# Optimization experiments

Measured on AMD Instinct MI355X. Metric: run time of the kernel, lower is better.

## Reference

```python
import jax, jax.numpy as jnp
import numpy as np

N = 20000          # nodes
E = 320000         # edges (avg degree 16)
FS = 1000          # feature_size (resnet feature width)
IN = 250 + FS + 250 + 85 * 3  # 1755, actual concat width


def setup_inputs() -> dict:
    key = jax.random.key(0)
    ks = jax.random.split(key, 16)
    # structured node feature matrix x: [layer_id | resnet(1000) | rel_size | rgb(3)]
    layer = jax.random.randint(ks[0], (N, 1), 1, 4).astype(jnp.float32)      # {1,2,3}
    resnet = jax.random.normal(ks[1], (N, FS), jnp.float32)
    rel = jax.random.uniform(ks[2], (N, 1), jnp.float32)                      # [0,1] -> idx 0..10
    colors = jax.random.randint(ks[3], (N, 3), 0, 256).astype(jnp.float32)
    x = jnp.concatenate([layer, resnet, rel, colors], axis=1)  # [N,1005]
    edge_index = jax.random.randint(ks[4], (2, E), 0, N)
    edge_attr = jax.random.uniform(ks[5], (E,), jnp.float32)

    def lin(k, fi, fo):
        return jax.random.normal(k, (fi, fo), jnp.float32) / np.sqrt(fi).astype(np.float32)

    return {
        "x": x,
        "edge_index": edge_index,
        "edge_attr": edge_attr,
        "layer_table": jax.random.normal(ks[6], (3, 250), jnp.float32),
        "rel_table": jax.random.normal(ks[7], (11, 250), jnp.float32),
        "color_table": jax.random.normal(ks[8], (256, 85), jnp.float32),
        "W1": lin(ks[9], IN, 512), "b1": jnp.zeros((512,), jnp.float32),
        "W2": lin(ks[10], 512, 256), "b2": jnp.zeros((256,), jnp.float32),
        "W3": lin(ks[11], 256, 64), "b3": jnp.zeros((64,), jnp.float32),
        "Wp": lin(ks[12], 64, 3), "bp": jnp.zeros((3,), jnp.float32),
    }


def _gcn_conv(h, src, dst, ew, W, b):
    # PyG GCNConv: h' = D^{-1/2} (A + I) D^{-1/2} (h W) + b, with edge weights ew
    h = h @ W
    deg = jax.ops.segment_sum(ew, dst, num_segments=N) + 1.0  # +1 for self-loop weight
    dinv = jnp.where(deg > 0.0, jax.lax.rsqrt(deg), 0.0)
    norm = dinv[src] * ew * dinv[dst]                          # [E]
    agg = jax.ops.segment_sum(h[src] * norm[:, None], dst, num_segments=N)
    agg = agg + h * (dinv * dinv)[:, None]                     # self-loop term
    return agg + b


def reference(x, edge_index, edge_attr, layer_table, rel_table, color_table,
              W1, b1, W2, b2, W3, b3, Wp, bp):
    src, dst = edge_index[0], edge_index[1]
    li = (x[:, 0] - 1.0).astype(jnp.int32)                      # layer id 0..2
    le = layer_table[li]                                        # [N,250]
    resnet = x[:, 1:FS + 1]                                     # [N,1000]
    ri = jnp.round(jnp.abs(x[:, FS + 1]) * 10.0).astype(jnp.int32)
    re = rel_table[ri]                                          # [N,250]
    ci = x[:, -3:].astype(jnp.int32)
    ce = color_table[ci].reshape(x.shape[0], -1)                # [N,255]
    h = jnp.concatenate([le, resnet, re, ce], axis=1)           # [N,1755]

    lrelu = lambda v: jax.nn.leaky_relu(v, 0.01)
    h = lrelu(_gcn_conv(h, src, dst, edge_attr, W1, b1))
    h = lrelu(_gcn_conv(h, src, dst, edge_attr, W2, b2))
    h = lrelu(_gcn_conv(h, src, dst, edge_attr, W3, b3))
    return h @ Wp + bp                                          # [N,3]
```

## Files before the change

kernel.cpp:

```cpp
#include <hip/hip_runtime.h>
#include <hip/hip_bf16.h>

#define NNODES 20000
#define NEDGES 320000
#define XW 1005
#define MP 20096

typedef __attribute__((ext_vector_type(8))) short short8;
typedef __attribute__((ext_vector_type(4))) float f32x4;
typedef __attribute__((ext_vector_type(4))) unsigned short u16x4;

typedef const __attribute__((address_space(1))) short8* g8cp;

__device__ inline void split1(float v, unsigned short& h, unsigned short& l) {
    unsigned u = __float_as_uint(v);
    h = (unsigned short)(u >> 16);
    float hf = __uint_as_float(u & 0xffff0000u);
    l = (unsigned short)(__float_as_uint(v - hf) >> 16);
}

#define PB_EDGE  1250
#define PB_IDX   1329
#define PB_A1    21329
#define PB_BT1   21841
#define PB_BT2   21969
#define PB_BT3   21985
#define PB_TAB   23549

__device__ inline void bt_split_body(int g, const float* __restrict__ W, int ldw,
                                     int koff, int K, int Kp, int Ncols,
                                     unsigned short* __restrict__ Bh,
                                     unsigned short* __restrict__ Bl) {
    int kp4 = Kp >> 2;
    if (g >= Ncols * kp4) return;
    int n = g / kp4, c4 = (g % kp4) << 2;
    u16x4 h, l;
#pragma unroll
    for (int i = 0; i < 4; ++i) {
        int k = c4 + i;
        float v = (k < K) ? W[(size_t)(koff + k) * ldw + n] : 0.0f;
        unsigned short hh, ll;
        split1(v, hh, ll);
        h[i] = (short)hh; l[i] = (short)ll;
    }
    *(u16x4*)&Bh[(size_t)n * Kp + c4] = h;
    *(u16x4*)&Bl[(size_t)n * Kp + c4] = l;
}

__global__ __launch_bounds__(256) void prep_kernel(
    const float* __restrict__ x, const int* __restrict__ ei, const float* __restrict__ ea,
    const float* __restrict__ layer_table, const float* __restrict__ rel_table,
    const float* __restrict__ color_table,
    const float* __restrict__ W1, const float* __restrict__ W2, const float* __restrict__ W3,
    float* __restrict__ deg, int* __restrict__ counts, int* __restrict__ idx8,
    unsigned short* __restrict__ A1h, unsigned short* __restrict__ A1l,
    unsigned short* __restrict__ Bt1h, unsigned short* __restrict__ Bt1l,
    unsigned short* __restrict__ Bt2h, unsigned short* __restrict__ Bt2l,
    unsigned short* __restrict__ Bt3h, unsigned short* __restrict__ Bt3l,
    float* __restrict__ T) {
    const int b = blockIdx.x;
    const int t = threadIdx.x;
    if (b < PB_EDGE) {
        int e = b * 256 + t;
        if (e >= NEDGES) return;
        int dst = ei[NEDGES + e];
        atomicAdd(&deg[dst], ea[e]);
        atomicAdd(&counts[dst], 1);
    } else if (b < PB_IDX) {
        int i = (b - PB_EDGE) * 256 + t;
        if (i >= NNODES) return;
        const float* r = x + (size_t)i * XW;
        idx8[i * 8 + 0] = (int)(r[0] - 1.0f);
        idx8[i * 8 + 1] = (int)rintf(fabsf(r[1001]) * 10.0f);
        idx8[i * 8 + 2] = (int)r[1002];
        idx8[i * 8 + 3] = (int)r[1003];
        idx8[i * 8 + 4] = (int)r[1004];
    } else if (b < PB_A1) {
        int row = b - PB_IDX;
        int c4 = t << 2;
        const float* xp = x + (size_t)row * XW + 1 + c4;
        u16x4 h, l;
#pragma unroll
        for (int i = 0; i < 4; ++i) {
            float v = (c4 + i < 1000) ? xp[i] : 0.0f;
            unsigned short hh, ll;
            split1(v, hh, ll);
            h[i] = (short)hh; l[i] = (short)ll;
        }
        *(u16x4*)&A1h[(size_t)row * 1024 + c4] = h;
        *(u16x4*)&A1l[(size_t)row * 1024 + c4] = l;
    } else if (b < PB_BT1) {
        bt_split_body((b - PB_A1) * 256 + t, W1, 512, 250, 1000, 1024, 512, Bt1h, Bt1l);
    } else if (b < PB_BT2) {
        bt_split_body((b - PB_BT1) * 256 + t, W2, 256, 0, 512, 512, 256, Bt2h, Bt2l);
    } else if (b < PB_BT3) {
        bt_split_body((b - PB_BT2) * 256 + t, W3, 64, 0, 256, 256, 64, Bt3h, Bt3l);
    } else {
        int g = (b - PB_BT3) * 256 + t;
        if (g >= 782 * 512) return;
        int row = g >> 9, col = g & 511;
        float acc = 0.0f;
        if (row < 3) {
            for (int k = 0; k < 250; ++k)
                acc += layer_table[row * 250 + k] * W1[(size_t)k * 512 + col];
        } else if (row < 14) {
            int r = row - 3;
            for (int k = 0; k < 250; ++k)
                acc += rel_table[r * 250 + k] * W1[(size_t)(1250 + k) * 512 + col];
        } else {
            int r = row - 14;
            int j = r >> 8, v = r & 255;
            int base = 1500 + 85 * j;
            for (int k = 0; k < 85; ++k)
                acc += color_table[v * 85 + k] * W1[(size_t)(base + k) * 512 + col];
        }
        T[(size_t)row * 512 + col] = acc;
    }
}


__global__ __launch_bounds__(1024) void scan_p1_kernel(const int* __restrict__ counts,
                                                       int* __restrict__ bsum,
                                                       const float* __restrict__ deg,
                                                       float* __restrict__ dinv, int n) {
    int b = blockIdx.x;
    if (b < 20) {
        __shared__ int ws[16];
        int t = threadIdx.x, lane = t & 63, wid = t >> 6;
        int i = b * 1024 + t;
        int v = (i < n) ? counts[i] : 0;
#pragma unroll
        for (int d = 32; d; d >>= 1) v += __shfl_down(v, d, 64);
        if (lane == 0) ws[wid] = v;
        __syncthreads();
        if (wid == 0) {
            int s = (lane < 16) ? ws[lane] : 0;
#pragma unroll
            for (int d = 8; d; d >>= 1) s += __shfl_down(s, d, 64);
            if (lane == 0) bsum[b] = s;
        }
    } else {
        int i = (b - 20) * 1024 + threadIdx.x;
        if (i < n) { float d = deg[i] + 1.0f; dinv[i] = 1.0f / sqrtf(d); }
    }
}

__global__ void scan_p2_kernel(const int* __restrict__ bsum, int* __restrict__ boffs,
                               int* __restrict__ offs, int n, int nb) {
    int lane = threadIdx.x;
    int v = (lane < nb) ? bsum[lane] : 0;
    int xv = v;
#pragma unroll
    for (int d = 1; d < 64; d <<= 1) {
        int u = __shfl_up(xv, d, 64);
        if (lane >= d) xv += u;
    }
    if (lane < nb) boffs[lane] = xv - v;
    if (lane == nb - 1) offs[n] = xv;
}

__global__ __launch_bounds__(1024) void scan_p3_kernel(const int* __restrict__ counts,
                                                       const int* __restrict__ boffs,
                                                       int* __restrict__ offs, int n) {
    __shared__ int wsum[16], wpre[16];
    int t = threadIdx.x, lane = t & 63, wid = t >> 6;
    int i = blockIdx.x * 1024 + t;
    int v = (i < n) ? counts[i] : 0;
    int xv = v;
#pragma unroll
    for (int d = 1; d < 64; d <<= 1) {
        int u = __shfl_up(xv, d, 64);
        if (lane >= d) xv += u;
    }
    if (lane == 63) wsum[wid] = xv;
    __syncthreads();
    if (wid == 0) {
        int s = (lane < 16) ? wsum[lane] : 0;
#pragma unroll
        for (int d = 1; d < 16; d <<= 1) {
            int u = __shfl_up(s, d, 64);
            if (lane >= d) s += u;
        }
        if (lane < 16) wpre[lane] = s;
    }
    __syncthreads();
    int prefix = boffs[blockIdx.x] + (wid > 0 ? wpre[wid - 1] : 0);
    if (i < n) offs[i] = prefix + xv - v;
}

__global__ void scatter_kernel(const int* __restrict__ ei, const float* __restrict__ ea,
                               const float* __restrict__ dinv, const int* __restrict__ offs,
                               int* __restrict__ cursor, int* __restrict__ csr_src,
                               float* __restrict__ csr_norm, int E) {
    int e = blockIdx.x * 256 + threadIdx.x;
    if (e >= E) return;
    int src = ei[e];
    int dst = ei[E + e];
    int slot = offs[dst] + atomicAdd(&cursor[dst], 1);
    csr_src[slot] = src;
    csr_norm[slot] = dinv[src] * ea[e] * dinv[dst];
}


template <int BN, int NCB, bool EMB>
__global__ __launch_bounds__(256, 3) void gemm_areg_kernel(
    const unsigned short* __restrict__ Ah, const unsigned short* __restrict__ Al, int Kp,
    const unsigned short* __restrict__ Bh, const unsigned short* __restrict__ Bl,
    float* __restrict__ C, int ldc, int M,
    const float* __restrict__ T, const int* __restrict__ idx8) {
    constexpr int NT = BN / 32;
    constexpr int BJ = BN / 64;
    __shared__ __align__(16) unsigned short sBh[2][BN * 32];
    __shared__ __align__(16) unsigned short sBl[2][BN * 32];

    const int t = threadIdx.x;
    const int lane = t & 63;
    const int w = t >> 6;
    const int wr = w >> 1, wc = w & 1;
    const int l15 = lane & 15, quad = lane >> 4;

    const int total = gridDim.x;
    const int per = total >> 3;
    const int bid = blockIdx.x;
    const int tile = (bid < (per << 3)) ? ((bid & 7) * per + (bid >> 3)) : bid;
    const int row0 = (tile / NCB) * 128;
    const int col0 = (tile % NCB) * BN;

    const int si_r = lane >> 2;
    const int si_s = lane & 3;
    const int schunk = si_s ^ ((si_r >> 1) & 3);
    const int sw = (quad ^ ((l15 >> 1) & 3)) * 8;

    const unsigned short* pAh[4]; const unsigned short* pAl[4];
#pragma unroll
    for (int mt = 0; mt < 4; ++mt) {
        int r = row0 + wr * 64 + mt * 16 + l15;
        size_t o = (size_t)r * Kp + quad * 8;
        pAh[mt] = Ah + o; pAl[mt] = Al + o;
    }

    const unsigned short* gB[BJ][2];
    int boff[BJ];
#pragma unroll
    for (int j = 0; j < BJ; ++j) {
        int rb = w * (BN / 4) + j * 16 + si_r;
        size_t e = (size_t)(col0 + rb) * Kp + schunk * 8;
        gB[j][0] = Bh + e; gB[j][1] = Bl + e;
        boff[j] = (w * (BN / 4) + j * 16 + si_r) * 32 + si_s * 8;
    }

    f32x4 acc[4][NT];
#pragma unroll
    for (int i = 0; i < 4; ++i)
#pragma unroll
        for (int j = 0; j < NT; ++j)
            acc[i][j] = (f32x4){0.f, 0.f, 0.f, 0.f};

    const int nit = Kp / 32;

    short8 a_h[4], a_l[4];
#pragma unroll
    for (int mt = 0; mt < 4; ++mt) {
        a_h[mt] = *(g8cp)(const void*)(pAh[mt]);
        a_l[mt] = *(g8cp)(const void*)(pAl[mt]);
    }
    short8 pB[BJ][2];
#pragma unroll
    for (int j = 0; j < BJ; ++j) {
        pB[j][0] = *(g8cp)(const void*)(gB[j][0]);
        pB[j][1] = *(g8cp)(const void*)(gB[j][1]);
    }
#pragma unroll
    for (int j = 0; j < BJ; ++j) {
        *(short8*)&sBh[0][boff[j]] = pB[j][0];
        *(short8*)&sBl[0][boff[j]] = pB[j][1];
    }
#pragma unroll
    for (int j = 0; j < BJ; ++j) {
        pB[j][0] = *(g8cp)(const void*)(gB[j][0] + 32);
        pB[j][1] = *(g8cp)(const void*)(gB[j][1] + 32);
    }
    __builtin_amdgcn_s_waitcnt(0xC07F);
    __builtin_amdgcn_s_barrier();
    __builtin_amdgcn_sched_barrier(0);

    for (int kt = 0; kt < nit; ++kt) {
        const int cur = kt & 1, nxt = cur ^ 1;
        const int kbn = (kt + 1 < nit) ? (kt + 1) * 32 : 0;
#pragma unroll
        for (int j = 0; j < BJ; ++j) {
            *(short8*)&sBh[nxt][boff[j]] = pB[j][0];
            *(short8*)&sBl[nxt][boff[j]] = pB[j][1];
        }
        {
            const int kb2 = (kt + 2 < nit) ? (kt + 2) * 32 : 0;
#pragma unroll
            for (int j = 0; j < BJ; ++j) {
                pB[j][0] = *(g8cp)(const void*)(gB[j][0] + kb2);
                pB[j][1] = *(g8cp)(const void*)(gB[j][1] + kb2);
            }
        }
        __builtin_amdgcn_s_waitcnt(0xC07F);
        __builtin_amdgcn_s_barrier();
        __builtin_amdgcn_sched_barrier(0);

        short8 fbh[NT], fbl[NT];
#pragma unroll
        for (int nt = 0; nt < NT; ++nt) {
            int off = (wc * (BN / 2) + nt * 16 + l15) * 32 + sw;
            fbh[nt] = *(const short8*)&sBh[cur][off];
            fbl[nt] = *(const short8*)&sBl[cur][off];
        }
#pragma unroll
        for (int mt = 0; mt < 4; ++mt) {
#pragma unroll
            for (int nt = 0; nt < NT; ++nt)
                acc[mt][nt] = __builtin_amdgcn_mfma_f32_16x16x32_bf16(a_h[mt], fbh[nt], acc[mt][nt], 0, 0, 0);
#pragma unroll
            for (int nt = 0; nt < NT; ++nt)
                acc[mt][nt] = __builtin_amdgcn_mfma_f32_16x16x32_bf16(a_h[mt], fbl[nt], acc[mt][nt], 0, 0, 0);
#pragma unroll
            for (int nt = 0; nt < NT; ++nt)
                acc[mt][nt] = __builtin_amdgcn_mfma_f32_16x16x32_bf16(a_l[mt], fbh[nt], acc[mt][nt], 0, 0, 0);
            a_h[mt] = *(g8cp)(const void*)(pAh[mt] + kbn);
            a_l[mt] = *(g8cp)(const void*)(pAl[mt] + kbn);
        }
    }

#pragma unroll
    for (int mt = 0; mt < 4; ++mt)
#pragma unroll
        for (int r = 0; r < 4; ++r) {
            int row = row0 + wr * 64 + mt * 16 + quad * 4 + r;
            if (row >= M) continue;
            if (EMB) {
                const int* ix = idx8 + row * 8;
                const float* t0 = T + (size_t)ix[0] * 512;
                const float* t1 = T + (size_t)(3 + ix[1]) * 512;
                const float* t2 = T + (size_t)(14 + ix[2]) * 512;
                const float* t3 = T + (size_t)(270 + ix[3]) * 512;
                const float* t4 = T + (size_t)(526 + ix[4]) * 512;
#pragma unroll
                for (int nt = 0; nt < NT; ++nt) {
                    int col = col0 + wc * (BN / 2) + nt * 16 + l15;
                    float e = t0[col] + t1[col] + t2[col] + t3[col] + t4[col];
                    C[(size_t)row * ldc + col] = acc[mt][nt][r] + e;
                }
            } else {
#pragma unroll
                for (int nt = 0; nt < NT; ++nt) {
                    int col = col0 + wc * (BN / 2) + nt * 16 + l15;
                    C[(size_t)row * ldc + col] = acc[mt][nt][r];
                }
            }
        }
}


template <int F, int CW, bool SPLIT, bool PROJ>
__global__ __launch_bounds__(256) void agg_cols_kernel(
    const float* __restrict__ H, const float* __restrict__ dinv,
    const int* __restrict__ offs, const int* __restrict__ csr_src,
    const float* __restrict__ csr_norm, const float* __restrict__ bias,
    float* __restrict__ outf, unsigned short* __restrict__ Hh,
    unsigned short* __restrict__ Hl,
    const float* __restrict__ Wp, const float* __restrict__ bp, int n_nodes) {
    constexpr int LPN = CW / 4;
    constexpr int NPB = 256 / LPN;
    constexpr int NCH = F / CW;
    constexpr int ECAP = 2048;
    __shared__ int   se[ECAP];
    __shared__ float sn[ECAP];

    const int chunk = blockIdx.x & (NCH - 1);
    const int nb    = blockIdx.x / NCH;
    const int n0 = nb * NPB;
    const int n1 = min(n0 + NPB, n_nodes);
    if (n0 >= n_nodes) return;

    const int estart = offs[n0];
    const int eend   = offs[n1];
    const int ecnt   = eend - estart;
    const bool inlds = (ecnt <= ECAP);
    if (inlds) {
        for (int i = threadIdx.x; i < ecnt; i += 256) {
            se[i] = csr_src[estart + i];
            sn[i] = csr_norm[estart + i];
        }
    }
    __syncthreads();

    const int n = n0 + threadIdx.x / LPN;
    if (n >= n_nodes) return;
    const int lane = threadIdx.x % LPN;
    const int c = chunk * CW + lane * 4;

    float di = dinv[n];
    float s = di * di;
    float4 h = *(const float4*)(H + (size_t)n * F + c);
    float4 acc = make_float4(h.x * s, h.y * s, h.z * s, h.w * s);
    int e0 = offs[n], e1 = offs[n + 1];
    if (inlds) {
        for (int e = e0 - estart; e < e1 - estart; ++e) {
            int src = se[e];
            float w = sn[e];
            float4 v = *(const float4*)(H + (size_t)src * F + c);
            acc.x += v.x * w; acc.y += v.y * w; acc.z += v.z * w; acc.w += v.w * w;
        }
    } else {
        for (int e = e0; e < e1; ++e) {
            int src = csr_src[e];
            float w = csr_norm[e];
            float4 v = *(const float4*)(H + (size_t)src * F + c);
            acc.x += v.x * w; acc.y += v.y * w; acc.z += v.z * w; acc.w += v.w * w;
        }
    }
    float4 b = *(const float4*)(bias + c);
    acc.x += b.x; acc.y += b.y; acc.z += b.z; acc.w += b.w;
    acc.x = acc.x > 0.f ? acc.x : 0.01f * acc.x;
    acc.y = acc.y > 0.f ? acc.y : 0.01f * acc.y;
    acc.z = acc.z > 0.f ? acc.z : 0.01f * acc.z;
    acc.w = acc.w > 0.f ? acc.w : 0.01f * acc.w;
    if (PROJ) {
        float p[3];
#pragma unroll
        for (int j = 0; j < 3; ++j)
            p[j] = acc.x * Wp[(c + 0) * 3 + j] + acc.y * Wp[(c + 1) * 3 + j] +
                   acc.z * Wp[(c + 2) * 3 + j] + acc.w * Wp[(c + 3) * 3 + j];
#pragma unroll
        for (int d = 1; d < LPN; d <<= 1) {
#pragma unroll
            for (int j = 0; j < 3; ++j)
                p[j] += __shfl_xor(p[j], d, 64);
        }
        if (lane == 0) {
#pragma unroll
            for (int j = 0; j < 3; ++j)
                outf[n * 3 + j] = p[j] + bp[j];
        }
    } else if (SPLIT) {
        u16x4 hh, ll;
        unsigned short a, bb;
        split1(acc.x, a, bb); hh[0] = (short)a; ll[0] = (short)bb;
        split1(acc.y, a, bb); hh[1] = (short)a; ll[1] = (short)bb;
        split1(acc.z, a, bb); hh[2] = (short)a; ll[2] = (short)bb;
        split1(acc.w, a, bb); hh[3] = (short)a; ll[3] = (short)bb;
        *(u16x4*)(Hh + (size_t)n * F + c) = hh;
        *(u16x4*)(Hl + (size_t)n * F + c) = ll;
    } else {
        *(float4*)(outf + (size_t)n * F + c) = acc;
    }
}


static inline size_t aln(size_t v) { return (v + 255) & ~(size_t)255; }

extern "C" void kernel_launch(void* const* d_in, const int* in_sizes, int n_in,
                              void* d_out, int out_size, void* d_ws, size_t ws_size,
                              hipStream_t stream) {
    const float* x           = (const float*)d_in[0];
    const int*   edge_index  = (const int*)d_in[1];
    const float* edge_attr   = (const float*)d_in[2];
    const float* layer_table = (const float*)d_in[3];
    const float* rel_table   = (const float*)d_in[4];
    const float* color_table = (const float*)d_in[5];
    const float* W1 = (const float*)d_in[6];
    const float* b1 = (const float*)d_in[7];
    const float* W2 = (const float*)d_in[8];
    const float* b2 = (const float*)d_in[9];
    const float* W3 = (const float*)d_in[10];
    const float* b3 = (const float*)d_in[11];
    const float* Wp = (const float*)d_in[12];
    const float* bp = (const float*)d_in[13];
    float* out = (float*)d_out;

    const int N = NNODES, E = NEDGES;

    char* p = (char*)d_ws;
    float* deg      = (float*)p;
    int*   counts   = (int*)(p + (size_t)N * 4);
    int*   cursor   = (int*)(p + (size_t)N * 8);     p += aln((size_t)N * 12);
    float* dinv     = (float*)p; p += aln((size_t)N * 4);
    float* T        = (float*)p; p += aln((size_t)782 * 512 * 4);
    float* csr_norm = (float*)p; p += aln((size_t)E * 4);
    float* C        = (float*)p; p += aln((size_t)MP * 512 * 4);
    unsigned short* BIG = (unsigned short*)p; p += aln((size_t)MP * 2048 * 2);
    unsigned short* Bt1h = (unsigned short*)p; p += aln((size_t)512 * 1024 * 2);
    unsigned short* Bt1l = (unsigned short*)p; p += aln((size_t)512 * 1024 * 2);
    unsigned short* Bt2h = (unsigned short*)p; p += aln((size_t)256 * 512 * 2);
    unsigned short* Bt2l = (unsigned short*)p; p += aln((size_t)256 * 512 * 2);
    unsigned short* Bt3h = (unsigned short*)p; p += aln((size_t)64 * 256 * 2);
    unsigned short* Bt3l = (unsigned short*)p; p += aln((size_t)64 * 256 * 2);
    int*   csr_src  = (int*)p;   p += aln((size_t)E * 4);
    int*   idx8     = (int*)p;   p += aln((size_t)N * 8 * 4);
    int*   offs     = (int*)p;   p += aln((size_t)(N + 1) * 4);
    int*   bsum     = (int*)p;   p += aln((size_t)32 * 4);
    int*   boffs    = (int*)p;   p += aln((size_t)32 * 4);

    unsigned short* A1h = BIG;
    unsigned short* A1l = BIG + (size_t)MP * 1024;
    unsigned short* H2h = BIG;
    unsigned short* H2l = BIG + (size_t)MP * 512;
    unsigned short* H3h = BIG + (size_t)MP * 1024;
    unsigned short* H3l = BIG + (size_t)MP * 1024 + (size_t)MP * 256;

    hipMemsetAsync(deg, 0, (size_t)N * 12, stream);

    prep_kernel<<<PB_TAB, 256, 0, stream>>>(
        x, edge_index, edge_attr, layer_table, rel_table, color_table,
        W1, W2, W3, deg, counts, idx8,
        A1h, A1l, Bt1h, Bt1l, Bt2h, Bt2l, Bt3h, Bt3l, T);

    scan_p1_kernel<<<40, 1024, 0, stream>>>(counts, bsum, deg, dinv, N);
    scan_p2_kernel<<<1, 64, 0, stream>>>(bsum, boffs, offs, N, 20);
    scan_p3_kernel<<<20, 1024, 0, stream>>>(counts, boffs, offs, N);
    scatter_kernel<<<(E + 255) / 256, 256, 0, stream>>>(edge_index, edge_attr, dinv, offs,
                                                        cursor, csr_src, csr_norm, E);

    const int nrb = MP / 128;

    {
        gemm_areg_kernel<128, 4, true><<<nrb * 4, 256, 0, stream>>>(
            A1h, A1l, 1024, Bt1h, Bt1l, C, 512, N, T, idx8);
        int nblocks = (N + 15) / 16;
        agg_cols_kernel<512, 64, true, false><<<8 * nblocks, 256, 0, stream>>>(
            C, dinv, offs, csr_src, csr_norm, b1, nullptr, H2h, H2l, nullptr, nullptr, N);
    }
    {
        gemm_areg_kernel<128, 2, false><<<nrb * 2, 256, 0, stream>>>(
            H2h, H2l, 512, Bt2h, Bt2l, C, 256, N, nullptr, nullptr);
        int nblocks = (N + 31) / 32;
        agg_cols_kernel<256, 32, true, false><<<8 * nblocks, 256, 0, stream>>>(
            C, dinv, offs, csr_src, csr_norm, b2, nullptr, H3h, H3l, nullptr, nullptr, N);
    }
    {
        gemm_areg_kernel<64, 1, false><<<nrb, 256, 0, stream>>>(
            H3h, H3l, 256, Bt3h, Bt3l, C, 64, N, nullptr, nullptr);
        int nblocks = (N + 15) / 16;
        agg_cols_kernel<64, 64, false, true><<<nblocks, 256, 0, stream>>>(
            C, dinv, offs, csr_src, csr_norm, b3, out, nullptr, nullptr, Wp, bp, N);
    }
}
```

Baseline: 527.0 us.

## Stage A tiles through shared memory with 64-row GEMM blocks

Replaces the GEMM kernel, which kept A fragments in registers loaded straight from global memory and double-buffered B in LDS, with a 64-row block tile. Both A and B are now staged through single-buffered LDS, and each wave computes a 32-row by BN/2 subtile. The smaller tile doubles the block count and cuts per-thread accumulator and register use, which is meant to raise occupancy and spread work better across CUs. In exchange it drops the B double buffering, adding a second barrier per k-step, and each B tile is reused over fewer rows, so more total B traffic is loaded.

```diff
diff --git a/kernel.cpp b/kernel.cpp
--- a/kernel.cpp
+++ b/kernel.cpp
@@ -203,15 +203,17 @@
 
 
 template <int BN, int NCB, bool EMB>
-__global__ __launch_bounds__(256, 3) void gemm_areg_kernel(
+__global__ __launch_bounds__(256, 3) void gemm_bm64_kernel(
     const unsigned short* __restrict__ Ah, const unsigned short* __restrict__ Al, int Kp,
     const unsigned short* __restrict__ Bh, const unsigned short* __restrict__ Bl,
     float* __restrict__ C, int ldc, int M,
     const float* __restrict__ T, const int* __restrict__ idx8) {
     constexpr int NT = BN / 32;
     constexpr int BJ = BN / 64;
-    __shared__ __align__(16) unsigned short sBh[2][BN * 32];
-    __shared__ __align__(16) unsigned short sBl[2][BN * 32];
+    __shared__ __align__(16) unsigned short sAh[64 * 32];
+    __shared__ __align__(16) unsigned short sAl[64 * 32];
+    __shared__ __align__(16) unsigned short sBh[BN * 32];
+    __shared__ __align__(16) unsigned short sBl[BN * 32];
 
     const int t = threadIdx.x;
     const int lane = t & 63;
@@ -223,7 +225,7 @@
     const int per = total >> 3;
     const int bid = blockIdx.x;
     const int tile = (bid < (per << 3)) ? ((bid & 7) * per + (bid >> 3)) : bid;
-    const int row0 = (tile / NCB) * 128;
+    const int row0 = (tile / NCB) * 64;
     const int col0 = (tile % NCB) * BN;
 
     const int si_r = lane >> 2;
@@ -231,14 +233,14 @@
     const int schunk = si_s ^ ((si_r >> 1) & 3);
     const int sw = (quad ^ ((l15 >> 1) & 3)) * 8;
 
-    const unsigned short* pAh[4]; const unsigned short* pAl[4];
-#pragma unroll
-    for (int mt = 0; mt < 4; ++mt) {
-        int r = row0 + wr * 64 + mt * 16 + l15;
-        size_t o = (size_t)r * Kp + quad * 8;
-        pAh[mt] = Ah + o; pAl[mt] = Al + o;
-    }
-
+    const unsigned short* gA[2];
+    int aoff;
+    {
+        int ra = w * 16 + si_r;
+        size_t e = (size_t)(row0 + ra) * Kp + schunk * 8;
+        gA[0] = Ah + e; gA[1] = Al + e;
+        aoff = (w * 16 + si_r) * 32 + si_s * 8;
+    }
     const unsigned short* gB[BJ][2];
     int boff[BJ];
 #pragma unroll
@@ -249,89 +251,82 @@
         boff[j] = (w * (BN / 4) + j * 16 + si_r) * 32 + si_s * 8;
     }
 
-    f32x4 acc[4][NT];
-#pragma unroll
-    for (int i = 0; i < 4; ++i)
+    f32x4 acc[2][NT];
+#pragma unroll
+    for (int i = 0; i < 2; ++i)
 #pragma unroll
         for (int j = 0; j < NT; ++j)
             acc[i][j] = (f32x4){0.f, 0.f, 0.f, 0.f};
 
     const int nit = Kp / 32;
 
-    short8 a_h[4], a_l[4];
-#pragma unroll
-    for (int mt = 0; mt < 4; ++mt) {
-        a_h[mt] = *(g8cp)(const void*)(pAh[mt]);
-        a_l[mt] = *(g8cp)(const void*)(pAl[mt]);
-    }
-    short8 pB[BJ][2];
+    short8 pA[2], pB[BJ][2];
+    pA[0] = *(g8cp)(const void*)(gA[0]);
+    pA[1] = *(g8cp)(const void*)(gA[1]);
 #pragma unroll
     for (int j = 0; j < BJ; ++j) {
         pB[j][0] = *(g8cp)(const void*)(gB[j][0]);
         pB[j][1] = *(g8cp)(const void*)(gB[j][1]);
     }
-#pragma unroll
-    for (int j = 0; j < BJ; ++j) {
-        *(short8*)&sBh[0][boff[j]] = pB[j][0];
-        *(short8*)&sBl[0][boff[j]] = pB[j][1];
-    }
-#pragma unroll
-    for (int j = 0; j < BJ; ++j) {
-        pB[j][0] = *(g8cp)(const void*)(gB[j][0] + 32);
-        pB[j][1] = *(g8cp)(const void*)(gB[j][1] + 32);
-    }
-    __builtin_amdgcn_s_waitcnt(0xC07F);
-    __builtin_amdgcn_s_barrier();
-    __builtin_amdgcn_sched_barrier(0);
 
     for (int kt = 0; kt < nit; ++kt) {
-        const int cur = kt & 1, nxt = cur ^ 1;
-        const int kbn = (kt + 1 < nit) ? (kt + 1) * 32 : 0;
+        *(short8*)&sAh[aoff] = pA[0];
+        *(short8*)&sAl[aoff] = pA[1];
 #pragma unroll
         for (int j = 0; j < BJ; ++j) {
-            *(short8*)&sBh[nxt][boff[j]] = pB[j][0];
-            *(short8*)&sBl[nxt][boff[j]] = pB[j][1];
-        }
-        {
-            const int kb2 = (kt + 2 < nit) ? (kt + 2) * 32 : 0;
+            *(short8*)&sBh[boff[j]] = pB[j][0];
+            *(short8*)&sBl[boff[j]] = pB[j][1];
+        }
+        if (kt + 1 < nit) {
+            const int kb = (kt + 1) * 32;
+            pA[0] = *(g8cp)(const void*)(gA[0] + kb);
+            pA[1] = *(g8cp)(const void*)(gA[1] + kb);
 #pragma unroll
             for (int j = 0; j < BJ; ++j) {
-                pB[j][0] = *(g8cp)(const void*)(gB[j][0] + kb2);
-                pB[j][1] = *(g8cp)(const void*)(gB[j][1] + kb2);
+                pB[j][0] = *(g8cp)(const void*)(gB[j][0] + kb);
+                pB[j][1] = *(g8cp)(const void*)(gB[j][1] + kb);
             }
         }
         __builtin_amdgcn_s_waitcnt(0xC07F);
         __builtin_amdgcn_s_barrier();
         __builtin_amdgcn_sched_barrier(0);
 
-        short8 fbh[NT], fbl[NT];
+        short8 fah[2], fal[2], fbh[NT], fbl[NT];
+#pragma unroll
+        for (int mt = 0; mt < 2; ++mt) {
+            int off = (wr * 32 + mt * 16 + l15) * 32 + sw;
+            fah[mt] = *(const short8*)&sAh[off];
+            fal[mt] = *(const short8*)&sAl[off];
+        }
 #pragma unroll
         for (int nt = 0; nt < NT; ++nt) {
             int off = (wc * (BN / 2) + nt * 16 + l15) * 32 + sw;
-            fbh[nt] = *(const short8*)&sBh[cur][off];
-            fbl[nt] = *(const short8*)&sBl[cur][off];
-        }
-#pragma unroll
-        for (int mt = 0; mt < 4; ++mt) {
+            fbh[nt] = *(const short8*)&sBh[off];
+            fbl[nt] = *(const short8*)&sBl[off];
+        }
+#pragma unroll
+        for (int mt = 0; mt < 2; ++mt)
 #pragma unroll
             for (int nt = 0; nt < NT; ++nt)
-                acc[mt][nt] = __builtin_amdgcn_mfma_f32_16x16x32_bf16(a_h[mt], fbh[nt], acc[mt][nt], 0, 0, 0);
+                acc[mt][nt] = __builtin_amdgcn_mfma_f32_16x16x32_bf16(fah[mt], fbh[nt], acc[mt][nt], 0, 0, 0);
+#pragma unroll
+        for (int mt = 0; mt < 2; ++mt)
 #pragma unroll
             for (int nt = 0; nt < NT; ++nt)
-                acc[mt][nt] = __builtin_amdgcn_mfma_f32_16x16x32_bf16(a_h[mt], fbl[nt], acc[mt][nt], 0, 0, 0);
+                acc[mt][nt] = __builtin_amdgcn_mfma_f32_16x16x32_bf16(fah[mt], fbl[nt], acc[mt][nt], 0, 0, 0);
+#pragma unroll
+        for (int mt = 0; mt < 2; ++mt)
 #pragma unroll
             for (int nt = 0; nt < NT; ++nt)
-                acc[mt][nt] = __builtin_amdgcn_mfma_f32_16x16x32_bf16(a_l[mt], fbh[nt], acc[mt][nt], 0, 0, 0);
-            a_h[mt] = *(g8cp)(const void*)(pAh[mt] + kbn);
-            a_l[mt] = *(g8cp)(const void*)(pAl[mt] + kbn);
-        }
-    }
-
-#pragma unroll
-    for (int mt = 0; mt < 4; ++mt)
+                acc[mt][nt] = __builtin_amdgcn_mfma_f32_16x16x32_bf16(fal[mt], fbh[nt], acc[mt][nt], 0, 0, 0);
+        if (kt + 1 < nit) __builtin_amdgcn_s_barrier();
+    }
+
+#pragma unroll
+    for (int mt = 0; mt < 2; ++mt)
 #pragma unroll
         for (int r = 0; r < 4; ++r) {
-            int row = row0 + wr * 64 + mt * 16 + quad * 4 + r;
+            int row = row0 + wr * 32 + mt * 16 + quad * 4 + r;
             if (row >= M) continue;
             if (EMB) {
                 const int* ix = idx8 + row * 8;
@@ -517,24 +512,24 @@
     scatter_kernel<<<(E + 255) / 256, 256, 0, stream>>>(edge_index, edge_attr, dinv, offs,
                                                         cursor, csr_src, csr_norm, E);
 
-    const int nrb = MP / 128;
+    const int nrb = MP / 64;
 
     {
-        gemm_areg_kernel<128, 4, true><<<nrb * 4, 256, 0, stream>>>(
+        gemm_bm64_kernel<128, 4, true><<<nrb * 4, 256, 0, stream>>>(
             A1h, A1l, 1024, Bt1h, Bt1l, C, 512, N, T, idx8);
         int nblocks = (N + 15) / 16;
         agg_cols_kernel<512, 64, true, false><<<8 * nblocks, 256, 0, stream>>>(
             C, dinv, offs, csr_src, csr_norm, b1, nullptr, H2h, H2l, nullptr, nullptr, N);
     }
     {
-        gemm_areg_kernel<128, 2, false><<<nrb * 2, 256, 0, stream>>>(
+        gemm_bm64_kernel<128, 2, false><<<nrb * 2, 256, 0, stream>>>(
             H2h, H2l, 512, Bt2h, Bt2l, C, 256, N, nullptr, nullptr);
         int nblocks = (N + 31) / 32;
         agg_cols_kernel<256, 32, true, false><<<8 * nblocks, 256, 0, stream>>>(
             C, dinv, offs, csr_src, csr_norm, b2, nullptr, H3h, H3l, nullptr, nullptr, N);
     }
     {
-        gemm_areg_kernel<64, 1, false><<<nrb, 256, 0, stream>>>(
+        gemm_bm64_kernel<64, 1, false><<<nrb, 256, 0, stream>>>(
             H3h, H3l, 256, Bt3h, Bt3l, C, 64, N, nullptr, nullptr);
         int nblocks = (N + 15) / 16;
         agg_cols_kernel<64, 64, false, true><<<nblocks, 256, 0, stream>>>(
```

After: 445.8 us. -15.4%, faster.
